# Performance work log

Hardware: AMD Instinct MI355X
Metric: run time of the kernel (lower is better)

The kernel has to match this reference:

```python
import jax, jax.numpy as jnp
import numpy as np
import math

B, H, S, D = 2, 16, 2048, 64

def setup_inputs() -> dict:
    key = jax.random.key(0)
    kq, kk, kv = jax.random.split(key, 3)
    Q = jax.random.normal(kq, (B, H, S, D), dtype=jnp.float32)
    K = jax.random.normal(kk, (B, H, S, D), dtype=jnp.float32)
    V = jax.random.normal(kv, (B, H, S, D), dtype=jnp.float32)
    causal_mask = jnp.tril(jnp.ones((S, S), dtype=bool))
    return {"Q": Q, "K": K, "V": V, "causal_mask": causal_mask}

def reference(Q, K, V, causal_mask):
    d_k = K.shape[-1]
    scores = jnp.einsum('bhqd,bhkd->bhqk', Q, K) / math.sqrt(d_k)
    scores = jnp.where(causal_mask, scores, -jnp.inf)
    probs = jax.nn.softmax(scores, axis=-1)
    return jnp.einsum('bhqk,bhkd->bhqd', probs, V)
```

## Files before the change

kernel.cpp:

```cpp
#include <hip/hip_runtime.h>
#include <math.h>


constexpr int kS   = 2048;
constexpr int kD   = 64;
constexpr int kBH  = 32;
constexpr int kPadP = 72;

typedef short short8 __attribute__((ext_vector_type(8)));
typedef float float4v __attribute__((ext_vector_type(4)));
typedef float float16v __attribute__((ext_vector_type(16)));
typedef unsigned int u32;
typedef unsigned short u16;

static __device__ inline u16 f2bf(float f) {
  union { float f; unsigned u; } v; v.f = f;
  unsigned r = v.u + 0x7FFF + ((v.u >> 16) & 1);
  return (u16)(r >> 16);
}

static __device__ inline short8 pack8(float4v a, float4v b) {
  short8 r;
  r[0] = (short)f2bf(a[0]); r[1] = (short)f2bf(a[1]);
  r[2] = (short)f2bf(a[2]); r[3] = (short)f2bf(a[3]);
  r[4] = (short)f2bf(b[0]); r[5] = (short)f2bf(b[1]);
  r[6] = (short)f2bf(b[2]); r[7] = (short)f2bf(b[3]);
  return r;
}

static __device__ inline void async_cp16(const void* g, void* l) {
  __builtin_amdgcn_global_load_lds(
      (const __attribute__((address_space(1))) u32*)g,
      (__attribute__((address_space(3))) u32*)l, 16, 0, 0);
}

static __device__ inline void swap32(u32 a, u32 b, u32& oa, u32& ob) {
#if __has_builtin(__builtin_amdgcn_permlane32_swap)
  auto r = __builtin_amdgcn_permlane32_swap(a, b, false, false);
  oa = r[0]; ob = r[1];
#else
  asm volatile("v_permlane32_swap_b32 %0, %1" : "+v"(a), "+v"(b));
  oa = a; ob = b;
#endif
}

__global__ __launch_bounds__(256)
void prep_kernel(const float* __restrict__ Q, const float* __restrict__ K,
                 const float* __restrict__ V,
                 u16* __restrict__ Qb, u16* __restrict__ Kb, u16* __restrict__ VT) {
  __shared__ u16 tile[64 * kPadP];
  const int tid = threadIdx.x;
  const int bh = blockIdx.y, st = blockIdx.x;
  const size_t ibase = (size_t)bh * kS * kD + (size_t)st * 64 * kD;
  const int r  = tid >> 2;
  const int c0 = (tid & 3) * 16;
  {
    const float scl = 0.125f * 1.44269504089f;
    const float* qp = Q + ibase + (size_t)r * kD + c0;
    float4v a = *(const float4v*)(qp);
    float4v b = *(const float4v*)(qp + 4);
    float4v c = *(const float4v*)(qp + 8);
    float4v d = *(const float4v*)(qp + 12);
    #pragma unroll
    for (int i = 0; i < 4; ++i) { a[i] *= scl; b[i] *= scl; c[i] *= scl; d[i] *= scl; }
    u16* dst = Qb + ibase + (size_t)r * kD + c0;
    *(short8*)dst       = pack8(a, b);
    *(short8*)(dst + 8) = pack8(c, d);
  }
  {
    const float* kp = K + ibase + (size_t)r * kD + c0;
    float4v a = *(const float4v*)(kp);
    float4v b = *(const float4v*)(kp + 4);
    float4v c = *(const float4v*)(kp + 8);
    float4v d = *(const float4v*)(kp + 12);
    u16* dst = Kb + ibase + (size_t)r * kD + c0;
    *(short8*)dst       = pack8(a, b);
    *(short8*)(dst + 8) = pack8(c, d);
  }
  {
    const float* vp = V + ibase + (size_t)r * kD + c0;
    float4v a = *(const float4v*)(vp);
    float4v b = *(const float4v*)(vp + 4);
    float4v c = *(const float4v*)(vp + 8);
    float4v d = *(const float4v*)(vp + 12);
    u16* t = &tile[r * kPadP + c0];
    *(short8*)t       = pack8(a, b);
    *(short8*)(t + 8) = pack8(c, d);
  }
  __syncthreads();
  {
    const int dd = tid >> 2;
    const int s0 = (tid & 3) * 16;
    short8 w0, w1;
    #pragma unroll
    for (int i = 0; i < 8; ++i) {
      w0[i] = (short)tile[(s0 + i) * kPadP + dd];
      w1[i] = (short)tile[(s0 + 8 + i) * kPadP + dd];
    }
    u16* vdst = VT + (size_t)bh * kD * kS + (size_t)dd * kS + st * 64 + s0;
    *(short8*)vdst       = w0;
    *(short8*)(vdst + 8) = w1;
  }
}

__global__ __launch_bounds__(256, 3)
void fattn_kernel(const u16* __restrict__ Qb, const u16* __restrict__ Kb,
                  const u16* __restrict__ VT, float* __restrict__ O) {
  __shared__ __align__(16) u16 ldsK[2][4096];
  __shared__ __align__(16) u16 ldsV[2][4096];

  const int tid  = threadIdx.x;
  const int wave = tid >> 6;
  const int lane = tid & 63;
  const int l31  = lane & 31;
  const int h    = lane >> 5;
  const int g    = wave & 1;
  const int kpar = wave >> 1;

  const int bh = blockIdx.y;
  const int qb = 31 - blockIdx.x;
  const int q0 = qb * 64;

  const size_t base  = (size_t)bh * kS * kD;
  const size_t vbase = (size_t)bh * kD * kS;

  const int lr  = lane >> 3;
  const int cxl = (lane & 7) ^ lr;
  const int offK0 = lr * 64   + cxl * 8;
  const int offV0 = lr * 2048 + cxl * 8;
  const unsigned hs16 = ((unsigned)(h ^ (l31 & 7))) * 16;

  float16v zf;
  #pragma unroll
  for (int i = 0; i < 16; ++i) zf[i] = 0.f;

  short8 qf[4];
  {
    const u16* qp = Qb + base + (size_t)(q0 + 32 * g + l31) * kD + h * 8;
    #pragma unroll
    for (int dk = 0; dk < 4; ++dk) qf[dk] = *(const short8*)(qp + dk * 16);
  }

  float16v acc0 = zf, acc1 = zf;
  float lac = 0.f;

  const int kmax = 2 * qb + g;

  {
    const u16* kg0 = Kb + base;
    const u16* vg0 = VT + vbase;
    #pragma unroll
    for (int j = 0; j < 2; ++j) {
      const int gg = wave + 4 * j;
      async_cp16(kg0 + gg * 512 + offK0,           &ldsK[0][gg * 512]);
      async_cp16(vg0 + (size_t)gg * 16384 + offV0, &ldsV[0][gg * 512]);
    }
  }

  for (int t = 0; t <= qb; ++t) {
    __syncthreads();
    if (t < qb) {
      const u16* kg0 = Kb + base + (size_t)(t + 1) * 4096;
      const u16* vg0 = VT + vbase + (t + 1) * 64;
      const int b = (t + 1) & 1;
      #pragma unroll
      for (int j = 0; j < 2; ++j) {
        const int gg = wave + 4 * j;
        async_cp16(kg0 + gg * 512 + offK0,           &ldsK[b][gg * 512]);
        async_cp16(vg0 + (size_t)gg * 16384 + offV0, &ldsV[b][gg * 512]);
      }
    }

    const int K32 = 2 * t + kpar;
    if (K32 <= kmax) {
      const char* KB = (const char*)ldsK[t & 1];
      const char* VB = (const char*)ldsV[t & 1];

      const char* krow = KB + (kpar * 32 + l31) * 128;
      short8 kf[4];
      #pragma unroll
      for (int dk = 0; dk < 4; ++dk)
        kf[dk] = *(const short8*)(krow + (((unsigned)(dk * 32)) ^ hs16));
      short8 vf[4];
      #pragma unroll
      for (int c = 0; c < 2; ++c) {
        const unsigned coff = ((unsigned)((kpar * 4 + 2 * c) * 16)) ^ hs16;
        vf[2 * c]     = *(const short8*)(VB + l31 * 128 + coff);
        vf[2 * c + 1] = *(const short8*)(VB + (32 + l31) * 128 + coff);
      }

      __builtin_amdgcn_s_setprio(1);
      float16v s = __builtin_amdgcn_mfma_f32_32x32x16_bf16(kf[0], qf[0], zf, 0, 0, 0);
      s = __builtin_amdgcn_mfma_f32_32x32x16_bf16(kf[1], qf[1], s, 0, 0, 0);
      s = __builtin_amdgcn_mfma_f32_32x32x16_bf16(kf[2], qf[2], s, 0, 0, 0);
      s = __builtin_amdgcn_mfma_f32_32x32x16_bf16(kf[3], qf[3], s, 0, 0, 0);
      __builtin_amdgcn_s_setprio(0);

      if (K32 == kmax) {
        const int ktb = t * 64 + kpar * 32;
        const int qg  = q0 + 32 * g + l31;
        #pragma unroll
        for (int r = 0; r < 16; ++r) {
          const int kg = ktb + (r & 3) + 8 * (r >> 2) + 4 * h;
          if (kg > qg) s[r] = -1e30f;
        }
      }

      u32 pk[8];
      #pragma unroll
      for (int g2 = 0; g2 < 4; ++g2) {
        const u32 u0 = __float_as_uint(__builtin_amdgcn_exp2f(s[4 * g2 + 0]));
        const u32 u1 = __float_as_uint(__builtin_amdgcn_exp2f(s[4 * g2 + 1]));
        const u32 u2 = __float_as_uint(__builtin_amdgcn_exp2f(s[4 * g2 + 2]));
        const u32 u3 = __float_as_uint(__builtin_amdgcn_exp2f(s[4 * g2 + 3]));
        pk[2 * g2]     = __builtin_amdgcn_perm(u1, u0, 0x07060302u);
        pk[2 * g2 + 1] = __builtin_amdgcn_perm(u3, u2, 0x07060302u);
      }

      {
        float e[8];
        #pragma unroll
        for (int i = 0; i < 8; ++i)
          e[i] = __uint_as_float(pk[i] << 16)
               + __uint_as_float(pk[i] & 0xFFFF0000u);
        e[0] += e[1]; e[2] += e[3]; e[4] += e[5]; e[6] += e[7];
        e[0] += e[2]; e[4] += e[6];
        lac += e[0] + e[4];
      }

      #pragma unroll
      for (int c = 0; c < 2; ++c) {
        const int ga = 4 * c, gb = 4 * c + 2;
        union { u32 u[4]; short8 s8; } pf;
        swap32(pk[ga],     pk[gb],     pf.u[0], pf.u[2]);
        swap32(pk[ga + 1], pk[gb + 1], pf.u[1], pf.u[3]);
        __builtin_amdgcn_s_setprio(1);
        acc0 = __builtin_amdgcn_mfma_f32_32x32x16_bf16(pf.s8, vf[2 * c],     acc0, 0, 0, 0);
        acc1 = __builtin_amdgcn_mfma_f32_32x32x16_bf16(pf.s8, vf[2 * c + 1], acc1, 0, 0, 0);
        __builtin_amdgcn_s_setprio(0);
      }
    }
  }

  __syncthreads();
  float* SA = (float*)&ldsK[0][0];
  float* SL = (float*)&ldsV[0][0];

  const float lt = lac + __shfl_xor(lac, 32);
  if (lane < 32) SL[kpar * 64 + g * 32 + lane] = lt;
  if (kpar == 1) {
    #pragma unroll
    for (int r = 0; r < 16; ++r) {
      const int row = (r & 3) + 8 * (r >> 2) + 4 * h;
      SA[(g * 32 + row) * 64 + l31]      = acc0[r];
      SA[(g * 32 + row) * 64 + 32 + l31] = acc1[r];
    }
  }
  __syncthreads();
  if (kpar == 0) {
    #pragma unroll
    for (int r = 0; r < 16; ++r) {
      const int row = (r & 3) + 8 * (r >> 2) + 4 * h;
      const float lsum = SL[g * 32 + row] + SL[64 + g * 32 + row];
      const float inv  = 1.f / lsum;
      const float o0 = (acc0[r] + SA[(g * 32 + row) * 64 + l31])      * inv;
      const float o1 = (acc1[r] + SA[(g * 32 + row) * 64 + 32 + l31]) * inv;
      float* op = O + ((size_t)bh * kS + q0 + 32 * g + row) * kD;
      op[l31]      = o0;
      op[l31 + 32] = o1;
    }
  }
}

extern "C" void kernel_launch(void* const* d_in, const int* in_sizes, int n_in,
                              void* d_out, int out_size, void* d_ws, size_t ws_size,
                              hipStream_t stream) {
  const float* Q = (const float*)d_in[0];
  const float* K = (const float*)d_in[1];
  const float* V = (const float*)d_in[2];
  float* O = (float*)d_out;

  const size_t nKV = (size_t)kBH * kS * kD;
  u16* Qb = (u16*)d_ws;
  u16* Kb = Qb + nKV;
  u16* VT = Kb + nKV;

  dim3 gprep(kS / 64, kBH);
  prep_kernel<<<gprep, 256, 0, stream>>>(Q, K, V, Qb, Kb, VT);
  dim3 grid(kS / 64, kBH);
  fattn_kernel<<<grid, 256, 0, stream>>>(Qb, Kb, VT, O);
}
```

Baseline: 150.0 us.

## Give each wave an independent 32-row query tile with balanced causal pairing

Drops the LDS double-buffered K/V staging and the cross-wave split-K reduction. Each wave now owns one 32-row query tile and streams K and V directly from global memory into registers, prefetching the next K block. Tiles are paired short-with-long within each block to balance causal work, and the grid shrinks to 16 blocks per head. The softmax row sum moves from VALU adds to an extra MFMA against a ones vector. In exchange it loses LDS reuse of K/V across waves, adds more global traffic per wave, and lowers the launch-bounds occupancy hint.

After: 165.9 us. 10.6% more time.

```diff
diff --git a/kernel.cpp b/kernel.cpp
--- a/kernel.cpp
+++ b/kernel.cpp
@@ -26,12 +26,6 @@
   r[4] = (short)f2bf(b[0]); r[5] = (short)f2bf(b[1]);
   r[6] = (short)f2bf(b[2]); r[7] = (short)f2bf(b[3]);
   return r;
-}
-
-static __device__ inline void async_cp16(const void* g, void* l) {
-  __builtin_amdgcn_global_load_lds(
-      (const __attribute__((address_space(1))) u32*)g,
-      (__attribute__((address_space(3))) u32*)l, 16, 0, 0);
 }
 
 static __device__ inline void swap32(u32 a, u32 b, u32& oa, u32& ob) {
@@ -103,172 +97,128 @@
   }
 }
 
-__global__ __launch_bounds__(256, 3)
+__global__ __launch_bounds__(256, 2)
 void fattn_kernel(const u16* __restrict__ Qb, const u16* __restrict__ Kb,
                   const u16* __restrict__ VT, float* __restrict__ O) {
-  __shared__ __align__(16) u16 ldsK[2][4096];
-  __shared__ __align__(16) u16 ldsV[2][4096];
-
   const int tid  = threadIdx.x;
   const int wave = tid >> 6;
   const int lane = tid & 63;
   const int l31  = lane & 31;
   const int h    = lane >> 5;
-  const int g    = wave & 1;
-  const int kpar = wave >> 1;
 
   const int bh = blockIdx.y;
-  const int qb = 31 - blockIdx.x;
-  const int q0 = qb * 64;
+  const int j  = blockIdx.x;
+
+  const int we = ((bh + j) & 1) ? (3 - wave) : wave;
+  const int s  = (we & 2) ? ((we & 1) ? 63 - j : 32 + j)
+                          : ((we & 1) ? 31 - j : j);
+  const int q0 = s * 32;
 
   const size_t base  = (size_t)bh * kS * kD;
   const size_t vbase = (size_t)bh * kD * kS;
 
-  const int lr  = lane >> 3;
-  const int cxl = (lane & 7) ^ lr;
-  const int offK0 = lr * 64   + cxl * 8;
-  const int offV0 = lr * 2048 + cxl * 8;
-  const unsigned hs16 = ((unsigned)(h ^ (l31 & 7))) * 16;
-
   float16v zf;
   #pragma unroll
   for (int i = 0; i < 16; ++i) zf[i] = 0.f;
 
+  short8 ones;
+  #pragma unroll
+  for (int i = 0; i < 8; ++i) ones[i] = (short)0x3F80;
+
   short8 qf[4];
   {
-    const u16* qp = Qb + base + (size_t)(q0 + 32 * g + l31) * kD + h * 8;
+    const u16* qp = Qb + base + (size_t)(q0 + l31) * kD + h * 8;
     #pragma unroll
     for (int dk = 0; dk < 4; ++dk) qf[dk] = *(const short8*)(qp + dk * 16);
   }
 
-  float16v acc0 = zf, acc1 = zf;
-  float lac = 0.f;
-
-  const int kmax = 2 * qb + g;
-
-  {
-    const u16* kg0 = Kb + base;
-    const u16* vg0 = VT + vbase;
-    #pragma unroll
-    for (int j = 0; j < 2; ++j) {
-      const int gg = wave + 4 * j;
-      async_cp16(kg0 + gg * 512 + offK0,           &ldsK[0][gg * 512]);
-      async_cp16(vg0 + (size_t)gg * 16384 + offV0, &ldsV[0][gg * 512]);
-    }
-  }
-
-  for (int t = 0; t <= qb; ++t) {
-    __syncthreads();
-    if (t < qb) {
-      const u16* kg0 = Kb + base + (size_t)(t + 1) * 4096;
-      const u16* vg0 = VT + vbase + (t + 1) * 64;
-      const int b = (t + 1) & 1;
+  const u16* kptr = Kb + base + (size_t)l31 * kD + h * 8;
+  const u16* vp0  = VT + vbase + (size_t)l31 * kS + h * 8;
+  const u16* vp1  = vp0 + (size_t)32 * kS;
+
+  float16v acc0 = zf, acc1 = zf, lacc = zf;
+
+  short8 kfA[4], kfB[4];
+  #pragma unroll
+  for (int dk = 0; dk < 4; ++dk) kfA[dk] = *(const short8*)(kptr + dk * 16);
+
+  const int qg = q0 + l31;
+
+  auto step = [&](short8* kfc, short8* kfn, int k) {
+    const u16* vk0 = vp0 + k * 32;
+    const u16* vk1 = vp1 + k * 32;
+    const short8 vf0 = *(const short8*)(vk0);
+    const short8 vf1 = *(const short8*)(vk1);
+    const short8 vf2 = *(const short8*)(vk0 + 16);
+    const short8 vf3 = *(const short8*)(vk1 + 16);
+    {
+      const int kn = (k < s) ? (k + 1) : k;
+      const u16* kp = kptr + (size_t)kn * 2048;
       #pragma unroll
-      for (int j = 0; j < 2; ++j) {
-        const int gg = wave + 4 * j;
-        async_cp16(kg0 + gg * 512 + offK0,           &ldsK[b][gg * 512]);
-        async_cp16(vg0 + (size_t)gg * 16384 + offV0, &ldsV[b][gg * 512]);
+      for (int dk = 0; dk < 4; ++dk) kfn[dk] = *(const short8*)(kp + dk * 16);
+    }
+
+    __builtin_amdgcn_s_setprio(1);
+    float16v sv = __builtin_amdgcn_mfma_f32_32x32x16_bf16(kfc[0], qf[0], zf, 0, 0, 0);
+    sv = __builtin_amdgcn_mfma_f32_32x32x16_bf16(kfc[1], qf[1], sv, 0, 0, 0);
+    sv = __builtin_amdgcn_mfma_f32_32x32x16_bf16(kfc[2], qf[2], sv, 0, 0, 0);
+    sv = __builtin_amdgcn_mfma_f32_32x32x16_bf16(kfc[3], qf[3], sv, 0, 0, 0);
+    __builtin_amdgcn_s_setprio(0);
+
+    if (k == s) {
+      #pragma unroll
+      for (int r = 0; r < 16; ++r) {
+        const int kg = k * 32 + (r & 3) + 8 * (r >> 2) + 4 * h;
+        if (kg > qg) sv[r] = -1e30f;
       }
     }
 
-    const int K32 = 2 * t + kpar;
-    if (K32 <= kmax) {
-      const char* KB = (const char*)ldsK[t & 1];
-      const char* VB = (const char*)ldsV[t & 1];
-
-      const char* krow = KB + (kpar * 32 + l31) * 128;
-      short8 kf[4];
-      #pragma unroll
-      for (int dk = 0; dk < 4; ++dk)
-        kf[dk] = *(const short8*)(krow + (((unsigned)(dk * 32)) ^ hs16));
-      short8 vf[4];
-      #pragma unroll
-      for (int c = 0; c < 2; ++c) {
-        const unsigned coff = ((unsigned)((kpar * 4 + 2 * c) * 16)) ^ hs16;
-        vf[2 * c]     = *(const short8*)(VB + l31 * 128 + coff);
-        vf[2 * c + 1] = *(const short8*)(VB + (32 + l31) * 128 + coff);
-      }
-
+    u32 pk[8];
+    #pragma unroll
+    for (int g2 = 0; g2 < 4; ++g2) {
+      const u32 u0 = __float_as_uint(__builtin_amdgcn_exp2f(sv[4 * g2 + 0]));
+      const u32 u1 = __float_as_uint(__builtin_amdgcn_exp2f(sv[4 * g2 + 1]));
+      const u32 u2 = __float_as_uint(__builtin_amdgcn_exp2f(sv[4 * g2 + 2]));
+      const u32 u3 = __float_as_uint(__builtin_amdgcn_exp2f(sv[4 * g2 + 3]));
+      pk[2 * g2]     = __builtin_amdgcn_perm(u1, u0, 0x07060302u);
+      pk[2 * g2 + 1] = __builtin_amdgcn_perm(u3, u2, 0x07060302u);
+    }
+
+    {
+      union { u32 u[4]; short8 s8; } pf;
+      swap32(pk[0], pk[2], pf.u[0], pf.u[2]);
+      swap32(pk[1], pk[3], pf.u[1], pf.u[3]);
       __builtin_amdgcn_s_setprio(1);
-      float16v s = __builtin_amdgcn_mfma_f32_32x32x16_bf16(kf[0], qf[0], zf, 0, 0, 0);
-      s = __builtin_amdgcn_mfma_f32_32x32x16_bf16(kf[1], qf[1], s, 0, 0, 0);
-      s = __builtin_amdgcn_mfma_f32_32x32x16_bf16(kf[2], qf[2], s, 0, 0, 0);
-      s = __builtin_amdgcn_mfma_f32_32x32x16_bf16(kf[3], qf[3], s, 0, 0, 0);
+      acc0 = __builtin_amdgcn_mfma_f32_32x32x16_bf16(pf.s8, vf0, acc0, 0, 0, 0);
+      acc1 = __builtin_amdgcn_mfma_f32_32x32x16_bf16(pf.s8, vf1, acc1, 0, 0, 0);
+      lacc = __builtin_amdgcn_mfma_f32_32x32x16_bf16(pf.s8, ones, lacc, 0, 0, 0);
       __builtin_amdgcn_s_setprio(0);
-
-      if (K32 == kmax) {
-        const int ktb = t * 64 + kpar * 32;
-        const int qg  = q0 + 32 * g + l31;
-        #pragma unroll
-        for (int r = 0; r < 16; ++r) {
-          const int kg = ktb + (r & 3) + 8 * (r >> 2) + 4 * h;
-          if (kg > qg) s[r] = -1e30f;
-        }
-      }
-
-      u32 pk[8];
-      #pragma unroll
-      for (int g2 = 0; g2 < 4; ++g2) {
-        const u32 u0 = __float_as_uint(__builtin_amdgcn_exp2f(s[4 * g2 + 0]));
-        const u32 u1 = __float_as_uint(__builtin_amdgcn_exp2f(s[4 * g2 + 1]));
-        const u32 u2 = __float_as_uint(__builtin_amdgcn_exp2f(s[4 * g2 + 2]));
-        const u32 u3 = __float_as_uint(__builtin_amdgcn_exp2f(s[4 * g2 + 3]));
-        pk[2 * g2]     = __builtin_amdgcn_perm(u1, u0, 0x07060302u);
-        pk[2 * g2 + 1] = __builtin_amdgcn_perm(u3, u2, 0x07060302u);
-      }
-
-      {
-        float e[8];
-        #pragma unroll
-        for (int i = 0; i < 8; ++i)
-          e[i] = __uint_as_float(pk[i] << 16)
-               + __uint_as_float(pk[i] & 0xFFFF0000u);
-        e[0] += e[1]; e[2] += e[3]; e[4] += e[5]; e[6] += e[7];
-        e[0] += e[2]; e[4] += e[6];
-        lac += e[0] + e[4];
-      }
-
-      #pragma unroll
-      for (int c = 0; c < 2; ++c) {
-        const int ga = 4 * c, gb = 4 * c + 2;
-        union { u32 u[4]; short8 s8; } pf;
-        swap32(pk[ga],     pk[gb],     pf.u[0], pf.u[2]);
-        swap32(pk[ga + 1], pk[gb + 1], pf.u[1], pf.u[3]);
-        __builtin_amdgcn_s_setprio(1);
-        acc0 = __builtin_amdgcn_mfma_f32_32x32x16_bf16(pf.s8, vf[2 * c],     acc0, 0, 0, 0);
-        acc1 = __builtin_amdgcn_mfma_f32_32x32x16_bf16(pf.s8, vf[2 * c + 1], acc1, 0, 0, 0);
-        __builtin_amdgcn_s_setprio(0);
-      }
-    }
-  }
-
-  __syncthreads();
-  float* SA = (float*)&ldsK[0][0];
-  float* SL = (float*)&ldsV[0][0];
-
-  const float lt = lac + __shfl_xor(lac, 32);
-  if (lane < 32) SL[kpar * 64 + g * 32 + lane] = lt;
-  if (kpar == 1) {
-    #pragma unroll
-    for (int r = 0; r < 16; ++r) {
-      const int row = (r & 3) + 8 * (r >> 2) + 4 * h;
-      SA[(g * 32 + row) * 64 + l31]      = acc0[r];
-      SA[(g * 32 + row) * 64 + 32 + l31] = acc1[r];
-    }
-  }
-  __syncthreads();
-  if (kpar == 0) {
-    #pragma unroll
-    for (int r = 0; r < 16; ++r) {
-      const int row = (r & 3) + 8 * (r >> 2) + 4 * h;
-      const float lsum = SL[g * 32 + row] + SL[64 + g * 32 + row];
-      const float inv  = 1.f / lsum;
-      const float o0 = (acc0[r] + SA[(g * 32 + row) * 64 + l31])      * inv;
-      const float o1 = (acc1[r] + SA[(g * 32 + row) * 64 + 32 + l31]) * inv;
-      float* op = O + ((size_t)bh * kS + q0 + 32 * g + row) * kD;
-      op[l31]      = o0;
-      op[l31 + 32] = o1;
-    }
+    }
+    {
+      union { u32 u[4]; short8 s8; } pf;
+      swap32(pk[4], pk[6], pf.u[0], pf.u[2]);
+      swap32(pk[5], pk[7], pf.u[1], pf.u[3]);
+      __builtin_amdgcn_s_setprio(1);
+      acc0 = __builtin_amdgcn_mfma_f32_32x32x16_bf16(pf.s8, vf2, acc0, 0, 0, 0);
+      acc1 = __builtin_amdgcn_mfma_f32_32x32x16_bf16(pf.s8, vf3, acc1, 0, 0, 0);
+      lacc = __builtin_amdgcn_mfma_f32_32x32x16_bf16(pf.s8, ones, lacc, 0, 0, 0);
+      __builtin_amdgcn_s_setprio(0);
+    }
+  };
+
+  int k = 0;
+  while (true) {
+    step(kfA, kfB, k); if (++k > s) break;
+    step(kfB, kfA, k); if (++k > s) break;
+  }
+
+  #pragma unroll
+  for (int r = 0; r < 16; ++r) {
+    const int row = (r & 3) + 8 * (r >> 2) + 4 * h;
+    const float inv = 1.f / lacc[r];
+    float* op = O + ((size_t)bh * kS + q0 + row) * kD;
+    op[l31]      = acc0[r] * inv;
+    op[l31 + 32] = acc1[r] * inv;
   }
 }
 
@@ -287,6 +237,6 @@
 
   dim3 gprep(kS / 64, kBH);
   prep_kernel<<<gprep, 256, 0, stream>>>(Q, K, V, Qb, Kb, VT);
-  dim3 grid(kS / 64, kBH);
+  dim3 grid(16, kBH);
   fattn_kernel<<<grid, 256, 0, stream>>>(Qb, Kb, VT, O);
 }
```
